# Kernel tuning notes

Measured on AMD Instinct MI355X. Metric: run time of the kernel, lower is better.

## Reference

```python
import jax, jax.numpy as jnp
import numpy as np
from jax import lax

EPS = 1e-6

def setup_inputs() -> dict:
    key = jax.random.key(0)
    B, C, K, T = 32, 1, 128, 8000
    x = jax.random.uniform(key, (B, C, K, T), dtype=jnp.float32)
    # parameters exactly as in PCENLayer.__init__ (log of init values)
    log_s = jnp.full((1, 1, K), np.log(0.025), dtype=jnp.float32)
    log_alpha = jnp.full((1, 1, K, 1), np.log(0.8), dtype=jnp.float32)
    log_delta = jnp.full((1, 1, K, 1), np.log(10.0), dtype=jnp.float32)
    log_r = jnp.full((1, 1, K, 1), np.log(0.25), dtype=jnp.float32)
    return {"x": x, "log_s": log_s, "log_alpha": log_alpha,
            "log_delta": log_delta, "log_r": log_r}

def reference(x, log_s, log_alpha, log_delta, log_r):
    # x: [B, C, K, T]
    s = jax.nn.sigmoid(log_s)            # (1, 1, K) smoother coefficient
    init = x[..., 0]                     # init smoother from first frame

    def step(prev, xt):
        f = (1.0 - s) * prev + s * xt
        return f, f

    xs = jnp.moveaxis(x[..., 1:], -1, 0)             # (T-1, B, C, K)
    _, fs = lax.scan(step, init, xs)                 # (T-1, B, C, K)
    filtered = jnp.concatenate([init[None], fs], 0)  # (T, B, C, K)
    filtered = jnp.moveaxis(filtered, 0, -1)         # (B, C, K, T)

    alpha = jnp.exp(log_alpha)           # (1, 1, K, 1)
    delta = jnp.exp(log_delta)
    r = jnp.exp(log_r)
    return (x / (EPS + filtered) ** alpha + delta) ** r - delta ** r
```

## Files before the change

kernel.cpp:

```cpp
#include <hip/hip_runtime.h>
#include <math.h>


constexpr int   T_LEN = 8000;
constexpr int   CHUNK = 16;
constexpr int   SEG   = 64 * CHUNK;
constexpr int   NSEG  = (T_LEN + SEG - 1) / SEG;
constexpr int   WARM  = 512;
constexpr int   WCH   = WARM / 64;
constexpr int   WPB   = 4;
constexpr int   NTH   = 64 * WPB;
constexpr int   KDIM  = 128;
constexpr float EPS_F = 1e-6f;
constexpr float LOG2E = 1.4426950408889634f;

typedef float f32x4 __attribute__((ext_vector_type(4)));

__global__ __launch_bounds__(NTH, 8) void pcen_kernel(
    const float* __restrict__ x,
    const float* __restrict__ log_s,
    const float* __restrict__ log_alpha,
    const float* __restrict__ log_delta,
    const float* __restrict__ log_r,
    float* __restrict__ out)
{
    const int tid  = threadIdx.x;
    const int lane = tid & 63;
    const int wave = tid >> 6;
    const int seq  = blockIdx.x >> 1;
    const int seg  = ((blockIdx.x & 1) << 2) + wave;
    const int k    = seq & (KDIM - 1);

    const float ls      = log_s[k];
    const float e_ns    = __builtin_amdgcn_exp2f(-ls * LOG2E);
    const float inv_s   = 1.0f + e_ns;
    const float s       = __builtin_amdgcn_rcpf(inv_s);
    const float a       = e_ns * s;
    const float alpha   = __builtin_amdgcn_exp2f(log_alpha[k] * LOG2E);
    const float delta   = __builtin_amdgcn_exp2f(log_delta[k] * LOG2E);
    const float r       = __builtin_amdgcn_exp2f(log_r[k] * LOG2E);
    const float delta_r = __builtin_amdgcn_exp2f(r * log_delta[k] * LOG2E);
    const float a2 = a * a, a4 = a2 * a2, a8 = a4 * a4, a16 = a8 * a8;

    const float* seq_base = x + (size_t)seq * T_LEN;
    const int    mbase    = seg * SEG + lane * CHUNK;
    const bool   active   = mbase < T_LEN;

    f32x4 w0 = {0,0,0,0}, w1 = {0,0,0,0};
    if (seg > 0) {
        const f32x4* wp = (const f32x4*)(seq_base + seg * SEG - WARM + lane * WCH);
        w0 = wp[0]; w1 = wp[1];
    }
    f32x4 xv[CHUNK / 4];
    if (active) {
        const f32x4* mp = (const f32x4*)(seq_base + mbase);
        #pragma unroll
        for (int v = 0; v < CHUNK / 4; ++v) xv[v] = mp[v];
    }

    float gin = 0.0f;
    if (seg > 0) {
        float gw = w0[0];
        gw = fmaf(a, gw, w0[1]); gw = fmaf(a, gw, w0[2]); gw = fmaf(a, gw, w0[3]);
        gw = fmaf(a, gw, w1[0]); gw = fmaf(a, gw, w1[1]);
        gw = fmaf(a, gw, w1[2]); gw = fmaf(a, gw, w1[3]);
        float Aw = a8, Bw = gw;
        #pragma unroll
        for (int off = 1; off < 64; off <<= 1) {
            const float pA = __shfl_up(Aw, off, 64);
            const float pB = __shfl_up(Bw, off, 64);
            if (lane >= off) { Bw = fmaf(Aw, pB, Bw); Aw = Aw * pA; }
        }
        gin = __shfl(Bw, 63, 64);
    }

    float A = 1.0f, B = 0.0f;
    if (active) {
        float g;
        if (seg == 0 && lane == 0) {
            g = xv[0][0] * inv_s;
            #pragma unroll
            for (int j = 1; j < CHUNK; ++j) g = fmaf(a, g, xv[j >> 2][j & 3]);
            A = 0.0f;
        } else {
            g = 0.0f;
            #pragma unroll
            for (int j = 0; j < CHUNK; ++j) g = fmaf(a, g, xv[j >> 2][j & 3]);
            A = a16;
        }
        B = g;
    }

    #pragma unroll
    for (int off = 1; off < 64; off <<= 1) {
        const float pA = __shfl_up(A, off, 64);
        const float pB = __shfl_up(B, off, 64);
        if (lane >= off) { B = fmaf(A, pB, B); A = A * pA; }
    }

    float eA = __shfl_up(A, 1, 64);
    float eB = __shfl_up(B, 1, 64);
    if (lane == 0) { eA = 1.0f; eB = 0.0f; }
    const float fin = fmaf(eA, gin, eB);

    if (active) {
        f32x4* op4 = (f32x4*)(out + (size_t)seq * T_LEN + mbase);
        float g = fin;
        #pragma unroll
        for (int v = 0; v < CHUNK / 4; ++v) {
            f32x4 ov;
            #pragma unroll
            for (int e = 0; e < 4; ++e) {
                const int   j  = 4 * v + e;
                const float xj = xv[v][e];
                if (j == 0 && seg == 0 && lane == 0) g = xj * inv_s;
                else                                 g = fmaf(a, g, xj);
                const float lg  = __builtin_amdgcn_logf(fmaf(s, g, EPS_F));
                const float inv = __builtin_amdgcn_exp2f(-alpha * lg);
                const float u   = fmaf(xj, inv, delta);
                ov[e] = __builtin_amdgcn_exp2f(r * __builtin_amdgcn_logf(u)) - delta_r;
            }
            op4[v] = ov;
        }
    }
}

extern "C" void kernel_launch(void* const* d_in, const int* in_sizes, int n_in,
                              void* d_out, int out_size, void* d_ws, size_t ws_size,
                              hipStream_t stream) {
    const float* x         = (const float*)d_in[0];
    const float* log_s     = (const float*)d_in[1];
    const float* log_alpha = (const float*)d_in[2];
    const float* log_delta = (const float*)d_in[3];
    const float* log_r     = (const float*)d_in[4];
    float* out = (float*)d_out;

    const int nseq    = in_sizes[0] / T_LEN;
    const int nblocks = nseq * 2;
    pcen_kernel<<<nblocks, NTH, 0, stream>>>(x, log_s, log_alpha, log_delta, log_r, out);
}
```

Measured before the change: 243.2 us.

## Assign one block per sequence with sequential subchunk scans and prefetch

```diff
diff --git a/kernel.cpp b/kernel.cpp
--- a/kernel.cpp
+++ b/kernel.cpp
@@ -3,11 +3,10 @@
 
 
 constexpr int   T_LEN = 8000;
-constexpr int   CHUNK = 16;
-constexpr int   SEG   = 64 * CHUNK;
-constexpr int   NSEG  = (T_LEN + SEG - 1) / SEG;
-constexpr int   WARM  = 512;
-constexpr int   WCH   = WARM / 64;
+constexpr int   CH    = 8;
+constexpr int   SUB   = 64 * CH;
+constexpr int   NSUB  = 4;
+constexpr int   WSEG  = SUB * NSUB;
 constexpr int   WPB   = 4;
 constexpr int   NTH   = 64 * WPB;
 constexpr int   KDIM  = 128;
@@ -24,11 +23,9 @@
     const float* __restrict__ log_r,
     float* __restrict__ out)
 {
-    const int tid  = threadIdx.x;
-    const int lane = tid & 63;
-    const int wave = tid >> 6;
-    const int seq  = blockIdx.x >> 1;
-    const int seg  = ((blockIdx.x & 1) << 2) + wave;
+    const int lane = threadIdx.x & 63;
+    const int wave = threadIdx.x >> 6;
+    const int seq  = blockIdx.x;
     const int k    = seq & (KDIM - 1);
 
     const float ls      = log_s[k];
@@ -40,88 +37,88 @@
     const float delta   = __builtin_amdgcn_exp2f(log_delta[k] * LOG2E);
     const float r       = __builtin_amdgcn_exp2f(log_r[k] * LOG2E);
     const float delta_r = __builtin_amdgcn_exp2f(r * log_delta[k] * LOG2E);
-    const float a2 = a * a, a4 = a2 * a2, a8 = a4 * a4, a16 = a8 * a8;
+    const float a2 = a * a, a4 = a2 * a2, a8 = a4 * a4;
 
-    const float* seq_base = x + (size_t)seq * T_LEN;
-    const int    mbase    = seg * SEG + lane * CHUNK;
-    const bool   active   = mbase < T_LEN;
+    const float* sb = x   + (size_t)seq * T_LEN;
+    float*       ob = out + (size_t)seq * T_LEN;
 
-    f32x4 w0 = {0,0,0,0}, w1 = {0,0,0,0};
-    if (seg > 0) {
-        const f32x4* wp = (const f32x4*)(seq_base + seg * SEG - WARM + lane * WCH);
-        w0 = wp[0]; w1 = wp[1];
-    }
-    f32x4 xv[CHUNK / 4];
-    if (active) {
-        const f32x4* mp = (const f32x4*)(seq_base + mbase);
-        #pragma unroll
-        for (int v = 0; v < CHUNK / 4; ++v) xv[v] = mp[v];
+
+    f32x4 bA[3], bB[3];
+
+    {
+        int b0 = wave * WSEG - SUB + lane * CH; if (b0 < 0) b0 = 0;
+        bA[0] = *(const f32x4*)(sb + b0);
+        bB[0] = *(const f32x4*)(sb + b0 + 4);
+        const int b1 = wave * WSEG + lane * CH;
+        bA[1] = *(const f32x4*)(sb + b1);
+        bB[1] = *(const f32x4*)(sb + b1 + 4);
     }
 
     float gin = 0.0f;
-    if (seg > 0) {
-        float gw = w0[0];
-        gw = fmaf(a, gw, w0[1]); gw = fmaf(a, gw, w0[2]); gw = fmaf(a, gw, w0[3]);
-        gw = fmaf(a, gw, w1[0]); gw = fmaf(a, gw, w1[1]);
-        gw = fmaf(a, gw, w1[2]); gw = fmaf(a, gw, w1[3]);
-        float Aw = a8, Bw = gw;
+
+    #pragma unroll
+    for (int t = 0; t <= NSUB; ++t) {
+        const int slot = t % 3;
+
+        if (t + 2 <= NSUB) {
+            const int slot2 = (t + 2) % 3;
+            const int b = wave * WSEG + (t + 1) * SUB + lane * CH;
+            if (b + CH <= T_LEN) {
+                bA[slot2] = *(const f32x4*)(sb + b);
+                bB[slot2] = *(const f32x4*)(sb + b + 4);
+            }
+        }
+
+        const int  eb  = wave * WSEG + (t - 1) * SUB + lane * CH;
+        const bool act = (t == 0) || (eb + CH <= T_LEN);
+
+        const float xs[CH] = { bA[slot][0], bA[slot][1], bA[slot][2], bA[slot][3],
+                               bB[slot][0], bB[slot][1], bB[slot][2], bB[slot][3] };
+
+        const bool absstart = (wave == 0) && (t == 1) && (lane == 0);
+        float A, B;
+        {
+            float g = absstart ? xs[0] * inv_s : xs[0];
+            #pragma unroll
+            for (int j = 1; j < CH; ++j) g = fmaf(a, g, xs[j]);
+            A = absstart ? 0.0f : a8;
+            B = g;
+            if (!act) { A = 1.0f; B = 0.0f; }
+        }
+
         #pragma unroll
         for (int off = 1; off < 64; off <<= 1) {
-            const float pA = __shfl_up(Aw, off, 64);
-            const float pB = __shfl_up(Bw, off, 64);
-            if (lane >= off) { Bw = fmaf(Aw, pB, Bw); Aw = Aw * pA; }
+            const float pA = __shfl_up(A, off, 64);
+            const float pB = __shfl_up(B, off, 64);
+            if (lane >= off) { B = fmaf(A, pB, B); A = A * pA; }
         }
-        gin = __shfl(Bw, 63, 64);
-    }
 
-    float A = 1.0f, B = 0.0f;
-    if (active) {
-        float g;
-        if (seg == 0 && lane == 0) {
-            g = xv[0][0] * inv_s;
+        float eA = __shfl_up(A, 1, 64);
+        float eB = __shfl_up(B, 1, 64);
+        if (lane == 0) { eA = 1.0f; eB = 0.0f; }
+        const float fin = fmaf(eA, gin, eB);
+        const float At  = __shfl(A, 63, 64);
+        const float Bt  = __shfl(B, 63, 64);
+
+        if (t >= 1 && act) {
+            f32x4 o0, o1;
+            float g = fin;
             #pragma unroll
-            for (int j = 1; j < CHUNK; ++j) g = fmaf(a, g, xv[j >> 2][j & 3]);
-            A = 0.0f;
-        } else {
-            g = 0.0f;
-            #pragma unroll
-            for (int j = 0; j < CHUNK; ++j) g = fmaf(a, g, xv[j >> 2][j & 3]);
-            A = a16;
-        }
-        B = g;
-    }
-
-    #pragma unroll
-    for (int off = 1; off < 64; off <<= 1) {
-        const float pA = __shfl_up(A, off, 64);
-        const float pB = __shfl_up(B, off, 64);
-        if (lane >= off) { B = fmaf(A, pB, B); A = A * pA; }
-    }
-
-    float eA = __shfl_up(A, 1, 64);
-    float eB = __shfl_up(B, 1, 64);
-    if (lane == 0) { eA = 1.0f; eB = 0.0f; }
-    const float fin = fmaf(eA, gin, eB);
-
-    if (active) {
-        f32x4* op4 = (f32x4*)(out + (size_t)seq * T_LEN + mbase);
-        float g = fin;
-        #pragma unroll
-        for (int v = 0; v < CHUNK / 4; ++v) {
-            f32x4 ov;
-            #pragma unroll
-            for (int e = 0; e < 4; ++e) {
-                const int   j  = 4 * v + e;
-                const float xj = xv[v][e];
-                if (j == 0 && seg == 0 && lane == 0) g = xj * inv_s;
-                else                                 g = fmaf(a, g, xj);
+            for (int j = 0; j < CH; ++j) {
+                const float xj = xs[j];
+                if (j == 0 && absstart) g = xj * inv_s;
+                else                    g = fmaf(a, g, xj);
                 const float lg  = __builtin_amdgcn_logf(fmaf(s, g, EPS_F));
                 const float inv = __builtin_amdgcn_exp2f(-alpha * lg);
                 const float u   = fmaf(xj, inv, delta);
-                ov[e] = __builtin_amdgcn_exp2f(r * __builtin_amdgcn_logf(u)) - delta_r;
+                const float ov  = __builtin_amdgcn_exp2f(r * __builtin_amdgcn_logf(u)) - delta_r;
+                if (j < 4) o0[j] = ov; else o1[j - 4] = ov;
             }
-            op4[v] = ov;
+            *(f32x4*)(ob + eb)     = o0;
+            *(f32x4*)(ob + eb + 4) = o1;
         }
+
+        gin = (t == 0 && wave == 0) ? 0.0f : fmaf(At, gin, Bt);
     }
 }
 
@@ -135,7 +132,6 @@
     const float* log_r     = (const float*)d_in[4];
     float* out = (float*)d_out;
 
-    const int nseq    = in_sizes[0] / T_LEN;
-    const int nblocks = nseq * 2;
-    pcen_kernel<<<nblocks, NTH, 0, stream>>>(x, log_s, log_alpha, log_delta, log_r, out);
+    const int nseq = in_sizes[0] / T_LEN;
+    pcen_kernel<<<nseq, NTH, 0, stream>>>(x, log_s, log_alpha, log_delta, log_r, out);
 }
```

Measured after the change: 240.3 us. About the same (-1.2%).
